# Kernel tuning notes

Measured on AMD Instinct MI355X. Metric: run time of the kernel, lower is better.

The kernel has to match this reference:

```python
import jax, jax.numpy as jnp
import numpy as np

N, L, E_Q, E_TOTAL, H, FORECAST = 4, 2048, 512, 512, 8, 8
E_HEAD = E_TOTAL // H
DT = 1.0
NEG = -1e30


def setup_inputs() -> dict:
    rng = jax.random.key(0)
    ks = jax.random.split(rng, 8)
    inv = 1.0 / np.sqrt(E_Q)
    return {
        "query": jax.random.normal(ks[0], (N, L, E_Q), jnp.float32),
        "key": jax.random.normal(ks[1], (N, L, E_Q), jnp.float32),
        "value": jax.random.normal(ks[2], (N, L, E_Q), jnp.float32),
        "Wqkv": jax.random.normal(ks[3], (E_Q, 3 * E_TOTAL), jnp.float32) * inv,
        "bqkv": jnp.zeros((3 * E_TOTAL,), jnp.float32),
        "Wo": jax.random.normal(ks[4], (E_TOTAL, E_Q), jnp.float32) * (1.0 / np.sqrt(E_TOTAL)),
        "bo": jnp.zeros((E_Q,), jnp.float32),
        "Xi": jax.random.normal(ks[5], (H, E_HEAD, E_HEAD), jnp.float32) * 0.02,
    }


def reference(query, key, value, Wqkv, bqkv, Wo, bo, Xi):
    # NOTE: original forward projects `query` into q,k,v (key/value args unused).
    b, s, _ = query.shape
    qkv = query @ Wqkv + bqkv                      # [b, s, 3E]
    q, k, v = jnp.split(qkv, 3, axis=-1)
    split_heads = lambda t: t.reshape(b, s, H, E_HEAD).transpose(0, 2, 1, 3)  # [b,H,s,h]
    q, k, v = split_heads(q), split_heads(k), split_heads(v)
    # causal SDPA
    scale = 1.0 / np.sqrt(E_HEAD)
    scores = jnp.einsum('bhqd,bhkd->bhqk', q, k) * scale
    causal = jnp.tril(jnp.ones((s, s), bool))
    scores = jnp.where(causal, scores, NEG)
    probs = jax.nn.softmax(scores, axis=-1)
    attn = jnp.einsum('bhqk,bhkd->bhqd', probs, v)  # [b,H,s,h]
    # per-head SINDy linear dynamics, strict symmetry -> skew-symmetric A
    A = Xi - jnp.swapaxes(Xi, -1, -2)               # [H,h,h]

    def step(x, _):
        x2 = x + DT * jnp.einsum('bhsd,hde->bhse', x, A)
        return x2, x2

    _, ys = jax.lax.scan(step, attn, None, length=FORECAST)  # [n,b,H,s,h]
    roll = jnp.transpose(ys, (1, 0, 3, 2, 4)).reshape(b, FORECAST, s, E_TOTAL)
    return roll @ Wo + bo                            # [b, n, s, E_q]
```

## Files before the change

kernel.cpp:

```cpp
#include <hip/hip_runtime.h>
#include <math.h>


#define NEGV -1e30f

typedef __bf16 bf16_t;
typedef __bf16 bf16x4 __attribute__((ext_vector_type(4)));
typedef __bf16 bf16x8 __attribute__((ext_vector_type(8)));
typedef float f32x4 __attribute__((ext_vector_type(4)));
typedef unsigned u32x4 __attribute__((ext_vector_type(4)));

#define MFMA(a, b, c) __builtin_amdgcn_mfma_f32_16x16x32_bf16((a), (b), (c), 0, 0, 0)

#define QSCALE 0.18033688011112042f

__device__ __forceinline__ bf16x8* swz_ptr(bf16_t* base, int r, int cb) {
  return (bf16x8*)((char*)base + r * 128 + (cb ^ ((r & 7) << 4)));
}
__device__ __forceinline__ const bf16x8* swz_cptr(const bf16_t* base, int r, int cb) {
  return (const bf16x8*)((const char*)base + r * 128 + (cb ^ ((r & 7) << 4)));
}

__device__ __forceinline__ void gload16(const bf16_t* g, bf16_t* l) {
  __builtin_amdgcn_global_load_lds(
      (const __attribute__((address_space(1))) void*)g,
      (__attribute__((address_space(3))) void*)l, 16, 0, 0);
}

__device__ __forceinline__ unsigned cvt_pk_bf16(float lo, float hi) {
  unsigned r;
  asm("v_cvt_pk_bf16_f32 %0, %1, %2" : "=v"(r) : "v"(lo), "v"(hi));
  return r;
}


__global__ __launch_bounds__(256) void prep(const float* __restrict__ X,
                                            const float* __restrict__ W,
                                            const float* __restrict__ Xi,
                                            bf16_t* __restrict__ Xb,
                                            bf16_t* __restrict__ WT,
                                            float* __restrict__ pows) {
  __shared__ __align__(16) char smem[2 * 64 * 68 * 4];
  const int bx = blockIdx.x;
  const int tid = threadIdx.x;
  if (bx < 8) {
    const int h = bx;
    float (*P)[68] = (float(*)[68])smem;
    float (*cur)[68] = (float(*)[68])(smem + 64 * 68 * 4);
    const float* xi = Xi + (size_t)h * 4096;
    float* dst = pows + (size_t)h * 8 * 4096;
    for (int idx = tid; idx < 4096; idx += 256) {
      const int i = idx >> 6, j = idx & 63;
      const float p = (i == j ? 1.f : 0.f) + xi[i * 64 + j] - xi[j * 64 + i];
      P[i][j] = p;
      cur[i][j] = p;
      dst[idx] = p;
    }
    __syncthreads();
    const int i = tid >> 2;
    const int j0 = (tid & 3) * 16;
    for (int n = 1; n < 8; ++n) {
      float a[16];
#pragma unroll
      for (int jj = 0; jj < 16; ++jj) a[jj] = 0.f;
      for (int dd = 0; dd < 64; ++dd) {
        const float c = cur[i][dd];
#pragma unroll
        for (int jj = 0; jj < 16; ++jj) a[jj] += c * P[dd][j0 + jj];
      }
      __syncthreads();
#pragma unroll
      for (int jj = 0; jj < 16; ++jj) {
        cur[i][j0 + jj] = a[jj];
        dst[n * 4096 + i * 64 + j0 + jj] = a[jj];
      }
      __syncthreads();
    }
  } else if (bx < 200) {
    const int idx = bx - 8;
    const int n0 = (idx % 24) * 64, k0 = (idx / 24) * 64;
    float (*Wf)[65] = (float(*)[65])smem;
#pragma unroll
    for (int c = 0; c < 16; ++c) {
      const int id2 = tid + c * 256;
      const int kk = id2 >> 6, nn = id2 & 63;
      Wf[kk][nn] = W[(size_t)(k0 + kk) * 1536 + n0 + nn];
    }
    __syncthreads();
    const int nr = tid >> 2;
    const int jb = (tid & 3) * 2;
#pragma unroll
    for (int t = 0; t < 2; ++t) {
      const int j = jb + t;
      bf16x8 v;
#pragma unroll
      for (int i = 0; i < 8; ++i) v[i] = (bf16_t)Wf[j * 8 + i][nr];
      *(bf16x8*)&WT[(size_t)(n0 + nr) * 512 + k0 + 8 * (j ^ (nr & 7))] = v;
    }
  } else {
    const int gid = (bx - 200) * 256 + tid;
    const int s = gid >> 6, j = gid & 63;
    const float4* src = (const float4*)(X + (size_t)s * 512 + j * 8);
    const float4 f0 = src[0], f1 = src[1];
    bf16x8 v;
    v[0] = (bf16_t)f0.x; v[1] = (bf16_t)f0.y; v[2] = (bf16_t)f0.z; v[3] = (bf16_t)f0.w;
    v[4] = (bf16_t)f1.x; v[5] = (bf16_t)f1.y; v[6] = (bf16_t)f1.z; v[7] = (bf16_t)f1.w;
    *(bf16x8*)&Xb[(size_t)s * 512 + (j >> 3) * 64 + 8 * ((j & 7) ^ (s & 7))] = v;
  }
}

__global__ __launch_bounds__(256) void build_B(const float* __restrict__ pows,
                                               const float* __restrict__ Wo,
                                               bf16_t* __restrict__ BmatT) {
  const int et = blockIdx.x;
  const int n = blockIdx.y;
  const int h = blockIdx.z;
  __shared__ __align__(16) float P[64][68];
  __shared__ __align__(16) float We[64][128];
  const int tid = threadIdx.x;
  const float* src = pows + ((size_t)h * 8 + n) * 4096;
  for (int idx = tid; idx < 4096; idx += 256) P[idx >> 6][idx & 63] = src[idx];
  const int e0 = et * 128;
  for (int idx = tid; idx < 8192; idx += 256) {
    const int dd = idx >> 7, e = idx & 127;
    We[dd][e] = Wo[(size_t)(h * 64 + dd) * 512 + e0 + e];
  }
  __syncthreads();
  const int d = tid >> 2;
  const int eq = (tid & 3) * 32;
  float acc[32];
#pragma unroll
  for (int j = 0; j < 32; ++j) acc[j] = 0.f;
  for (int dd = 0; dd < 64; ++dd) {
    const float p = P[d][dd];
#pragma unroll
    for (int j = 0; j < 32; ++j) acc[j] += p * We[dd][eq + j];
  }
  bf16_t* dst = BmatT + (size_t)n * 512 * 512 + (size_t)(e0 + eq) * 512 + h * 64;
  const int dlo = d & 7, dhi = d >> 3;
#pragma unroll
  for (int j = 0; j < 32; ++j)
    dst[(size_t)j * 512 + 8 * (dhi ^ (j & 7)) + dlo] = (bf16_t)acc[j];
}

__global__ __launch_bounds__(256) void qkv_gemm(const bf16_t* __restrict__ Xb,
                                                const bf16_t* __restrict__ WT,
                                                const float* __restrict__ bias,
                                                bf16_t* __restrict__ qw,
                                                bf16_t* __restrict__ kw,
                                                bf16_t* __restrict__ vt) {
  __shared__ __align__(16) bf16_t As[2][128 * 64];
  __shared__ __align__(16) bf16_t Bs[2][128 * 64];
  const int tid = threadIdx.x;
  const int wave = tid >> 6, lane = tid & 63;
  const int g = lane >> 4, li = lane & 15;
  const int row0 = blockIdx.x * 128;
  const int col0 = blockIdx.y * 128;
  const int wm = (wave >> 1) * 64, wn = (wave & 1) * 64;
  f32x4 acc[4][4] = {};
  const bf16_t* asrc = Xb + (size_t)(row0 + wave * 32 + (lane >> 3)) * 512 + (lane & 7) * 8;
  const bf16_t* bsrc = WT + (size_t)(col0 + wave * 32 + (lane >> 3)) * 512 + (lane & 7) * 8;
  bf16_t* adst0 = &As[0][wave * 32 * 64];
  bf16_t* adst1 = &As[1][wave * 32 * 64];
  bf16_t* bdst0 = &Bs[0][wave * 32 * 64];
  bf16_t* bdst1 = &Bs[1][wave * 32 * 64];
  auto stage = [&](int bi, int kt) {
    const int k0 = kt * 64;
    bf16_t* ad = bi ? adst1 : adst0;
    bf16_t* bd = bi ? bdst1 : bdst0;
#pragma unroll
    for (int c = 0; c < 4; ++c) {
      gload16(asrc + (size_t)c * 8 * 512 + k0, ad + c * 512);
      gload16(bsrc + (size_t)c * 8 * 512 + k0, bd + c * 512);
    }
  };
  stage(0, 0);
#pragma unroll
  for (int t = 0; t < 8; ++t) {
    const int cur = t & 1;
    if (t < 7) {
      stage(cur ^ 1, t + 1);
      asm volatile("s_waitcnt vmcnt(8)" ::: "memory");
    } else {
      asm volatile("s_waitcnt vmcnt(0)" ::: "memory");
    }
    __builtin_amdgcn_s_barrier();
    __builtin_amdgcn_sched_barrier(0);
#pragma unroll
    for (int ks = 0; ks < 2; ++ks) {
      bf16x8 af[4], bfr[4];
#pragma unroll
      for (int mr = 0; mr < 4; ++mr)
        af[mr] = *swz_cptr(As[cur], wm + mr * 16 + li, ks * 64 + g * 16);
#pragma unroll
      for (int nr = 0; nr < 4; ++nr)
        bfr[nr] = *swz_cptr(Bs[cur], wn + nr * 16 + li, ks * 64 + g * 16);
#pragma unroll
      for (int mr = 0; mr < 4; ++mr)
#pragma unroll
        for (int nr = 0; nr < 4; ++nr)
          acc[mr][nr] = MFMA(af[mr], bfr[nr], acc[mr][nr]);
    }
    __builtin_amdgcn_s_barrier();
    __builtin_amdgcn_sched_barrier(0);
  }
  const int cbase = col0 + wn;
  const int sel = cbase >> 9;
  const int hh = (cbase & 511) >> 6;
  const int bb = row0 >> 11;
  const size_t hb = (size_t)(bb * 8 + hh) * (2048 * 64);
  if (sel == 2) {
    bf16_t* vbase = vt + hb;
#pragma unroll
    for (int nr = 0; nr < 4; ++nr) {
      const int dcol = nr * 16 + li;
      const float bv = bias[cbase + dcol];
#pragma unroll
      for (int mr = 0; mr < 4; ++mr) {
        bf16x4 pk;
#pragma unroll
        for (int i = 0; i < 4; ++i) pk[i] = (bf16_t)(acc[mr][nr][i] + bv);
        const int s = (row0 + wm + mr * 16 + g * 4) & 2047;
        *(bf16x4*)&vbase[(size_t)dcol * 2048 + s] = pk;
      }
    }
  } else {
    bf16_t* dstp = (sel == 0 ? qw : kw) + hb;
    const float sc = (sel == 0) ? QSCALE : 1.0f;
#pragma unroll
    for (int nr = 0; nr < 4; ++nr) {
      const int dcol = nr * 16 + li;
      const float bv = bias[cbase + dcol];
#pragma unroll
      for (int mr = 0; mr < 4; ++mr) {
#pragma unroll
        for (int i = 0; i < 4; ++i) {
          const int r = row0 + wm + mr * 16 + g * 4 + i;
          const int s = r & 2047;
          dstp[(size_t)s * 64 + dcol] = (bf16_t)((acc[mr][nr][i] + bv) * sc);
        }
      }
    }
  }
}

__global__ __launch_bounds__(256) void fattn(const bf16_t* __restrict__ qw,
                                             const bf16_t* __restrict__ kw,
                                             const bf16_t* __restrict__ vt,
                                             bf16_t* __restrict__ attn,
                                             float* __restrict__ opart,
                                             float* __restrict__ ml) {
  __shared__ __align__(16) bf16_t Ks[2][64][64];
  __shared__ __align__(16) bf16_t Vs[2][64][64];
  const int tid = threadIdx.x;
  const int w = tid >> 6;
  const int lane = tid & 63;
  const int g = lane >> 4;
  const int li = lane & 15;
  const int x = blockIdx.x;
  int qt, ktb, kte, chunk;
  bool split;
  if (x < 16) {
    qt = 31 - x; ktb = 0; kte = 16; chunk = 0; split = true;
  } else if (x < 32) {
    qt = 47 - x; ktb = 16; kte = qt + 1; chunk = 1; split = true;
  } else {
    qt = 47 - x; ktb = 0; kte = qt + 1; chunk = 0; split = false;
  }
  const int h = blockIdx.y;
  const int b = blockIdx.z;
  const size_t base = ((size_t)(b * 8 + h)) * (2048 * 64);
  const int q0 = qt * 64;
  const int qrow = q0 + w * 16 + li;
  const bf16x8 aq0 = *(const bf16x8*)(qw + base + (size_t)qrow * 64 + g * 8);
  const bf16x8 aq1 = *(const bf16x8*)(qw + base + (size_t)qrow * 64 + 32 + g * 8);
  const bf16_t* kbase = kw + base;
  const bf16_t* vbase = vt + base;
  const int r_st = tid >> 2;
  const int qu = tid & 3;
  {
    const bf16_t* kp = kbase + (size_t)(ktb * 64 + r_st) * 64 + qu * 16;
    const bf16_t* vp = vbase + (size_t)r_st * 2048 + ktb * 64 + qu * 16;
    *swz_ptr(&Ks[0][0][0], r_st, qu * 32) = *(const bf16x8*)kp;
    *swz_ptr(&Ks[0][0][0], r_st, qu * 32 + 16) = *(const bf16x8*)(kp + 8);
    *swz_ptr(&Vs[0][0][0], r_st, qu * 32) = *(const bf16x8*)vp;
    *swz_ptr(&Vs[0][0][0], r_st, qu * 32 + 16) = *(const bf16x8*)(vp + 8);
  }
  f32x4 accO[4] = {};
  float m_run = -__builtin_inff();
  float l_run = 0.f;
  for (int kt = ktb; kt < kte; ++kt) {
    __syncthreads();
    const int cur = (kt - ktb) & 1;
    const bool pf = (kt + 1) < kte;
    bf16x8 nk0, nk1, nv0, nv1;
    if (pf) {
      const int kb2 = (kt + 1) * 64;
      const bf16_t* kp = kbase + (size_t)(kb2 + r_st) * 64 + qu * 16;
      const bf16_t* vp = vbase + (size_t)r_st * 2048 + kb2 + qu * 16;
      nk0 = *(const bf16x8*)kp;
      nk1 = *(const bf16x8*)(kp + 8);
      nv0 = *(const bf16x8*)vp;
      nv1 = *(const bf16x8*)(vp + 8);
    }
    f32x4 sv[4];
    __builtin_amdgcn_s_setprio(1);
#pragma unroll
    for (int nt = 0; nt < 4; ++nt) {
      const bf16x8 bk0 = *swz_cptr(&Ks[cur][0][0], nt * 16 + li, g * 16);
      const bf16x8 bk1 = *swz_cptr(&Ks[cur][0][0], nt * 16 + li, 64 + g * 16);
      f32x4 z = {0.f, 0.f, 0.f, 0.f};
      z = MFMA(bk0, aq0, z);
      sv[nt] = MFMA(bk1, aq1, z);
    }
    __builtin_amdgcn_s_setprio(0);
    if (kt == qt) {
#pragma unroll
      for (int nt = 0; nt < 4; ++nt)
#pragma unroll
        for (int i = 0; i < 4; ++i)
          if (nt * 16 + g * 4 + i > w * 16 + li) sv[nt][i] = NEGV;
    }
    float pmax = sv[0][0];
#pragma unroll
    for (int nt = 0; nt < 4; ++nt)
#pragma unroll
      for (int i = 0; i < 4; ++i) pmax = fmaxf(pmax, sv[nt][i]);
    pmax = fmaxf(pmax, __shfl_xor(pmax, 16, 64));
    pmax = fmaxf(pmax, __shfl_xor(pmax, 32, 64));
    if (!__all(pmax - m_run <= 8.f)) {
      const float newm = fmaxf(m_run, pmax);
      const float sc = exp2f(m_run - newm);
      l_run *= sc;
      m_run = newm;
#pragma unroll
      for (int nt = 0; nt < 4; ++nt)
#pragma unroll
        for (int i = 0; i < 4; ++i) accO[nt][i] *= sc;
    }
    float rsum = 0.f;
#pragma unroll
    for (int nt = 0; nt < 4; ++nt) {
#pragma unroll
      for (int i = 0; i < 4; ++i) {
        const float p = exp2f(sv[nt][i] - m_run);
        sv[nt][i] = p;
        rsum += p;
      }
    }
    rsum += __shfl_xor(rsum, 16, 64);
    rsum += __shfl_xor(rsum, 32, 64);
    l_run += rsum;
    const unsigned pk00 = cvt_pk_bf16(sv[0][0], sv[0][1]);
    const unsigned pk01 = cvt_pk_bf16(sv[0][2], sv[0][3]);
    const unsigned pk10 = cvt_pk_bf16(sv[1][0], sv[1][1]);
    const unsigned pk11 = cvt_pk_bf16(sv[1][2], sv[1][3]);
    const unsigned pk20 = cvt_pk_bf16(sv[2][0], sv[2][1]);
    const unsigned pk21 = cvt_pk_bf16(sv[2][2], sv[2][3]);
    const unsigned pk30 = cvt_pk_bf16(sv[3][0], sv[3][1]);
    const unsigned pk31 = cvt_pk_bf16(sv[3][2], sv[3][3]);
    bf16x8 ap0, ap1;
    {
      auto s0 = __builtin_amdgcn_permlane32_swap((int)pk00, (int)pk10, false, false);
      auto t0 = __builtin_amdgcn_permlane16_swap(s0[0], s0[1], false, false);
      auto s1 = __builtin_amdgcn_permlane32_swap((int)pk01, (int)pk11, false, false);
      auto t1 = __builtin_amdgcn_permlane16_swap(s1[0], s1[1], false, false);
      u32x4 wd = {(unsigned)t0[0], (unsigned)t1[0], (unsigned)t0[1], (unsigned)t1[1]};
      ap0 = __builtin_bit_cast(bf16x8, wd);
    }
    {
      auto s0 = __builtin_amdgcn_permlane32_swap((int)pk20, (int)pk30, false, false);
      auto t0 = __builtin_amdgcn_permlane16_swap(s0[0], s0[1], false, false);
      auto s1 = __builtin_amdgcn_permlane32_swap((int)pk21, (int)pk31, false, false);
      auto t1 = __builtin_amdgcn_permlane16_swap(s1[0], s1[1], false, false);
      u32x4 wd = {(unsigned)t0[0], (unsigned)t1[0], (unsigned)t0[1], (unsigned)t1[1]};
      ap1 = __builtin_bit_cast(bf16x8, wd);
    }
    __builtin_amdgcn_s_setprio(1);
#pragma unroll
    for (int nt = 0; nt < 4; ++nt) {
      const bf16x8 bv0 = *swz_cptr(&Vs[cur][0][0], nt * 16 + li, g * 16);
      const bf16x8 bv1 = *swz_cptr(&Vs[cur][0][0], nt * 16 + li, 64 + g * 16);
      accO[nt] = MFMA(bv0, ap0, accO[nt]);
      accO[nt] = MFMA(bv1, ap1, accO[nt]);
    }
    __builtin_amdgcn_s_setprio(0);
    if (pf) {
      *swz_ptr(&Ks[cur ^ 1][0][0], r_st, qu * 32) = nk0;
      *swz_ptr(&Ks[cur ^ 1][0][0], r_st, qu * 32 + 16) = nk1;
      *swz_ptr(&Vs[cur ^ 1][0][0], r_st, qu * 32) = nv0;
      *swz_ptr(&Vs[cur ^ 1][0][0], r_st, qu * 32 + 16) = nv1;
    }
  }
  if (!split) {
    const float inv = 1.0f / l_run;
    bf16_t* arow = attn + (size_t)(b * 2048 + qrow) * 512 + h * 64;
#pragma unroll
    for (int nt = 0; nt < 4; ++nt) {
      bf16x4 pk;
#pragma unroll
      for (int i = 0; i < 4; ++i) pk[i] = (bf16_t)(accO[nt][i] * inv);
      *(bf16x4*)&arow[8 * ((nt * 2 + (g >> 1)) ^ (li & 7)) + (g & 1) * 4] = pk;
    }
  } else {
    const int row = w * 16 + li;
    const size_t pbase = (((size_t)(b * 8 + h) * 16 + (qt - 16)) * 2 + chunk) * 64 + row;
    float* op = opart + pbase * 64;
#pragma unroll
    for (int nt = 0; nt < 4; ++nt) *(f32x4*)&op[nt * 16 + g * 4] = accO[nt];
    if (g == 0) {
      ml[pbase * 2] = m_run;
      ml[pbase * 2 + 1] = l_run;
    }
  }
}

__global__ __launch_bounds__(256) void fcombine(const float* __restrict__ opart,
                                                const float* __restrict__ ml,
                                                bf16_t* __restrict__ attn) {
  const int qi = blockIdx.x;
  const int h = blockIdx.y;
  const int b = blockIdx.z;
  const int tid = threadIdx.x;
  const int row = tid >> 2;
  const int dq = (tid & 3) * 16;
  const size_t base2 = ((size_t)(b * 8 + h) * 16 + qi) * 2;
  const size_t p0 = (base2 * 64 + row);
  const size_t p1 = ((base2 + 1) * 64 + row);
  const float m1 = ml[p0 * 2], l1 = ml[p0 * 2 + 1];
  const float m2 = ml[p1 * 2], l2 = ml[p1 * 2 + 1];
  const float m = fmaxf(m1, m2);
  const float w1 = exp2f(m1 - m), w2 = exp2f(m2 - m);
  const float inv = 1.0f / (l1 * w1 + l2 * w2);
  const float* o1 = opart + p0 * 64;
  const float* o2 = opart + p1 * 64;
  const int qrow = (16 + qi) * 64 + row;
  bf16_t* arow = attn + (size_t)(b * 2048 + qrow) * 512 + h * 64;
#pragma unroll
  for (int t = 0; t < 2; ++t) {
    const int c0 = dq + t * 8;
    const f32x4 a1 = *(const f32x4*)&o1[c0];
    const f32x4 b1 = *(const f32x4*)&o1[c0 + 4];
    const f32x4 a2 = *(const f32x4*)&o2[c0];
    const f32x4 b2 = *(const f32x4*)&o2[c0 + 4];
    bf16x8 v;
#pragma unroll
    for (int i = 0; i < 4; ++i) {
      v[i] = (bf16_t)((a1[i] * w1 + a2[i] * w2) * inv);
      v[4 + i] = (bf16_t)((b1[i] * w1 + b2[i] * w2) * inv);
    }
    *(bf16x8*)&arow[8 * ((c0 >> 3) ^ (row & 7))] = v;
  }
}

__global__ __launch_bounds__(256) void out_gemm(const bf16_t* __restrict__ A,
                                                const bf16_t* __restrict__ BmatT,
                                                const float* __restrict__ bo,
                                                float* __restrict__ out) {
  __shared__ __align__(16) bf16_t As[2][128 * 64];
  const int tid = threadIdx.x;
  const int wave = tid >> 6, lane = tid & 63;
  const int g = lane >> 4, li = lane & 15;
  const int row0 = blockIdx.x * 128;
  const int col0 = blockIdx.y * 128;
  const int nf = blockIdx.z;
  const int wm = (wave >> 1) * 64, wn = (wave & 1) * 64;
  f32x4 acc[4][4] = {};
  const bf16_t* asrc = A + (size_t)(row0 + wave * 32 + (lane >> 3)) * 512 + (lane & 7) * 8;
  bf16_t* adst0 = &As[0][wave * 32 * 64];
  bf16_t* adst1 = &As[1][wave * 32 * 64];
  const char* Bnf = (const char*)(BmatT + (size_t)nf * 512 * 512);
  unsigned boff[2][4];
#pragma unroll
  for (int ks = 0; ks < 2; ++ks)
#pragma unroll
    for (int nr = 0; nr < 4; ++nr) {
      const int row = col0 + wn + nr * 16 + li;
      boff[ks][nr] = (unsigned)(row * 1024 + 16 * ((ks * 4 + g) ^ (row & 7)));
    }
  auto stageA = [&](int bi, int kt) {
    bf16_t* ad = bi ? adst1 : adst0;
#pragma unroll
    for (int c = 0; c < 4; ++c)
      gload16(asrc + (size_t)c * 8 * 512 + kt * 64, ad + c * 512);
  };
  bf16x8 bfr[2][2][4];
  auto loadB = [&](int bi, int kt) {
#pragma unroll
    for (int ks = 0; ks < 2; ++ks)
#pragma unroll
      for (int nr = 0; nr < 4; ++nr)
        bfr[bi][ks][nr] = *(const bf16x8*)(Bnf + boff[ks][nr] + kt * 128);
  };
  stageA(0, 0);
  loadB(0, 0);
#pragma unroll
  for (int t = 0; t < 8; ++t) {
    const int cur = t & 1;
    if (t < 7) {
      stageA(cur ^ 1, t + 1);
      loadB(cur ^ 1, t + 1);
      asm volatile("s_waitcnt vmcnt(12)" ::: "memory");
    } else {
      asm volatile("s_waitcnt vmcnt(0)" ::: "memory");
    }
    __builtin_amdgcn_s_barrier();
    __builtin_amdgcn_sched_barrier(0);
#pragma unroll
    for (int ks = 0; ks < 2; ++ks) {
      bf16x8 af[4];
#pragma unroll
      for (int mr = 0; mr < 4; ++mr)
        af[mr] = *swz_cptr(As[cur], wm + mr * 16 + li, ks * 64 + g * 16);
#pragma unroll
      for (int mr = 0; mr < 4; ++mr)
#pragma unroll
        for (int nr = 0; nr < 4; ++nr)
          acc[mr][nr] = MFMA(af[mr], bfr[cur][ks][nr], acc[mr][nr]);
    }
    __builtin_amdgcn_s_barrier();
    __builtin_amdgcn_sched_barrier(0);
  }
  const int bb = row0 >> 11;
  float* obase = out + ((size_t)(bb * 8 + nf)) * (2048 * 512);
#pragma unroll
  for (int nr = 0; nr < 4; ++nr) {
    const int c = col0 + wn + nr * 16 + li;
    const float bv = bo[c];
#pragma unroll
    for (int mr = 0; mr < 4; ++mr) {
#pragma unroll
      for (int i = 0; i < 4; ++i) {
        const int r = row0 + wm + mr * 16 + g * 4 + i;
        const int s = r & 2047;
        __builtin_nontemporal_store(acc[mr][nr][i] + bv, &obase[(size_t)s * 512 + c]);
      }
    }
  }
}

extern "C" void kernel_launch(void* const* d_in, const int* in_sizes, int n_in,
                              void* d_out, int out_size, void* d_ws, size_t ws_size,
                              hipStream_t stream) {
  const float* query = (const float*)d_in[0];
  const float* Wqkv = (const float*)d_in[3];
  const float* bqkv = (const float*)d_in[4];
  const float* Wo = (const float*)d_in[5];
  const float* bo = (const float*)d_in[6];
  const float* Xi = (const float*)d_in[7];
  float* out = (float*)d_out;

  char* ws = (char*)d_ws;
  bf16_t* qw = (bf16_t*)(ws + 0);
  bf16_t* kw = (bf16_t*)(ws + 8388608);
  bf16_t* vt = (bf16_t*)(ws + 16777216);
  bf16_t* Xb = (bf16_t*)(ws + 25165824);
  bf16_t* attn = (bf16_t*)(ws + 25165824);
  bf16_t* BmatT = (bf16_t*)(ws + 33554432);
  float* pows = (float*)(ws + 37748736);
  bf16_t* WT = (bf16_t*)(ws + 38797312);
  float* opart = (float*)(ws + 40370176);
  float* mlbuf = (float*)(ws + 57147392);

  prep<<<dim3(2248), dim3(256), 0, stream>>>(query, Wqkv, Xi, Xb, WT, pows);
  build_B<<<dim3(4, 8, 8), dim3(256), 0, stream>>>(pows, Wo, BmatT);
  qkv_gemm<<<dim3(64, 12), dim3(256), 0, stream>>>(Xb, WT, bqkv, qw, kw, vt);
  fattn<<<dim3(48, 8, 4), dim3(256), 0, stream>>>(qw, kw, vt, attn, opart, mlbuf);
  fcombine<<<dim3(16, 8, 4), dim3(256), 0, stream>>>(opart, mlbuf, attn);
  out_gemm<<<dim3(64, 4, 8), dim3(256), 0, stream>>>(attn, BmatT, bo, out);
}
```

Baseline: 181.1 us.

## Process 128 query rows per attention block to reuse K/V tiles across two row groups

```diff
diff --git a/kernel.cpp b/kernel.cpp
--- a/kernel.cpp
+++ b/kernel.cpp
@@ -258,22 +258,26 @@
   const int g = lane >> 4;
   const int li = lane & 15;
   const int x = blockIdx.x;
-  int qt, ktb, kte, chunk;
+  int qt2, ktb, kte, chunk;
   bool split;
-  if (x < 16) {
-    qt = 31 - x; ktb = 0; kte = 16; chunk = 0; split = true;
-  } else if (x < 32) {
-    qt = 47 - x; ktb = 16; kte = qt + 1; chunk = 1; split = true;
+  if (x < 8) {
+    qt2 = 15 - x; ktb = 0; kte = qt2 + 1; chunk = 0; split = true;
+  } else if (x < 16) {
+    qt2 = 23 - x; ktb = qt2 + 1; kte = 2 * qt2 + 2; chunk = 1; split = true;
   } else {
-    qt = 47 - x; ktb = 0; kte = qt + 1; chunk = 0; split = false;
+    qt2 = 23 - x; ktb = 0; kte = 2 * qt2 + 2; chunk = 0; split = false;
   }
   const int h = blockIdx.y;
   const int b = blockIdx.z;
   const size_t base = ((size_t)(b * 8 + h)) * (2048 * 64);
-  const int q0 = qt * 64;
-  const int qrow = q0 + w * 16 + li;
-  const bf16x8 aq0 = *(const bf16x8*)(qw + base + (size_t)qrow * 64 + g * 8);
-  const bf16x8 aq1 = *(const bf16x8*)(qw + base + (size_t)qrow * 64 + 32 + g * 8);
+  const int rbase0 = qt2 * 128 + w * 32;
+  bf16x8 aq[2][2];
+#pragma unroll
+  for (int u = 0; u < 2; ++u) {
+    const bf16_t* qp = qw + base + (size_t)(rbase0 + u * 16 + li) * 64 + g * 8;
+    aq[u][0] = *(const bf16x8*)qp;
+    aq[u][1] = *(const bf16x8*)(qp + 32);
+  }
   const bf16_t* kbase = kw + base;
   const bf16_t* vbase = vt + base;
   const int r_st = tid >> 2;
@@ -286,16 +290,17 @@
     *swz_ptr(&Vs[0][0][0], r_st, qu * 32) = *(const bf16x8*)vp;
     *swz_ptr(&Vs[0][0][0], r_st, qu * 32 + 16) = *(const bf16x8*)(vp + 8);
   }
-  f32x4 accO[4] = {};
-  float m_run = -__builtin_inff();
-  float l_run = 0.f;
+  f32x4 accO[2][4] = {};
+  float m_run[2] = {-__builtin_inff(), -__builtin_inff()};
+  float l_run[2] = {0.f, 0.f};
   for (int kt = ktb; kt < kte; ++kt) {
     __syncthreads();
     const int cur = (kt - ktb) & 1;
     const bool pf = (kt + 1) < kte;
+    const int kb = kt * 64;
     bf16x8 nk0, nk1, nv0, nv1;
     if (pf) {
-      const int kb2 = (kt + 1) * 64;
+      const int kb2 = kb + 64;
       const bf16_t* kp = kbase + (size_t)(kb2 + r_st) * 64 + qu * 16;
       const bf16_t* vp = vbase + (size_t)r_st * 2048 + kb2 + qu * 16;
       nk0 = *(const bf16x8*)kp;
@@ -303,88 +308,97 @@
       nv0 = *(const bf16x8*)vp;
       nv1 = *(const bf16x8*)(vp + 8);
     }
-    f32x4 sv[4];
-    __builtin_amdgcn_s_setprio(1);
+    bf16x8 bk[8];
 #pragma unroll
     for (int nt = 0; nt < 4; ++nt) {
-      const bf16x8 bk0 = *swz_cptr(&Ks[cur][0][0], nt * 16 + li, g * 16);
-      const bf16x8 bk1 = *swz_cptr(&Ks[cur][0][0], nt * 16 + li, 64 + g * 16);
-      f32x4 z = {0.f, 0.f, 0.f, 0.f};
-      z = MFMA(bk0, aq0, z);
-      sv[nt] = MFMA(bk1, aq1, z);
-    }
-    __builtin_amdgcn_s_setprio(0);
-    if (kt == qt) {
+      bk[2 * nt] = *swz_cptr(&Ks[cur][0][0], nt * 16 + li, g * 16);
+      bk[2 * nt + 1] = *swz_cptr(&Ks[cur][0][0], nt * 16 + li, 64 + g * 16);
+    }
+#pragma unroll
+    for (int u = 0; u < 2; ++u) {
+      const int rbase = rbase0 + u * 16;
+      if (kb > rbase + 15) continue;
+      f32x4 sv[4];
+      __builtin_amdgcn_s_setprio(1);
+#pragma unroll
+      for (int nt = 0; nt < 4; ++nt) {
+        f32x4 z = {0.f, 0.f, 0.f, 0.f};
+        z = MFMA(bk[2 * nt], aq[u][0], z);
+        sv[nt] = MFMA(bk[2 * nt + 1], aq[u][1], z);
+      }
+      __builtin_amdgcn_s_setprio(0);
+      if (kb + 63 > rbase) {
+#pragma unroll
+        for (int nt = 0; nt < 4; ++nt)
+#pragma unroll
+          for (int i = 0; i < 4; ++i)
+            if (kb + nt * 16 + g * 4 + i > rbase + li) sv[nt][i] = NEGV;
+      }
+      float pmax = sv[0][0];
 #pragma unroll
       for (int nt = 0; nt < 4; ++nt)
 #pragma unroll
-        for (int i = 0; i < 4; ++i)
-          if (nt * 16 + g * 4 + i > w * 16 + li) sv[nt][i] = NEGV;
-    }
-    float pmax = sv[0][0];
-#pragma unroll
-    for (int nt = 0; nt < 4; ++nt)
-#pragma unroll
-      for (int i = 0; i < 4; ++i) pmax = fmaxf(pmax, sv[nt][i]);
-    pmax = fmaxf(pmax, __shfl_xor(pmax, 16, 64));
-    pmax = fmaxf(pmax, __shfl_xor(pmax, 32, 64));
-    if (!__all(pmax - m_run <= 8.f)) {
-      const float newm = fmaxf(m_run, pmax);
-      const float sc = exp2f(m_run - newm);
-      l_run *= sc;
-      m_run = newm;
-#pragma unroll
-      for (int nt = 0; nt < 4; ++nt)
-#pragma unroll
-        for (int i = 0; i < 4; ++i) accO[nt][i] *= sc;
-    }
-    float rsum = 0.f;
-#pragma unroll
-    for (int nt = 0; nt < 4; ++nt) {
-#pragma unroll
-      for (int i = 0; i < 4; ++i) {
-        const float p = exp2f(sv[nt][i] - m_run);
-        sv[nt][i] = p;
-        rsum += p;
-      }
-    }
-    rsum += __shfl_xor(rsum, 16, 64);
-    rsum += __shfl_xor(rsum, 32, 64);
-    l_run += rsum;
-    const unsigned pk00 = cvt_pk_bf16(sv[0][0], sv[0][1]);
-    const unsigned pk01 = cvt_pk_bf16(sv[0][2], sv[0][3]);
-    const unsigned pk10 = cvt_pk_bf16(sv[1][0], sv[1][1]);
-    const unsigned pk11 = cvt_pk_bf16(sv[1][2], sv[1][3]);
-    const unsigned pk20 = cvt_pk_bf16(sv[2][0], sv[2][1]);
-    const unsigned pk21 = cvt_pk_bf16(sv[2][2], sv[2][3]);
-    const unsigned pk30 = cvt_pk_bf16(sv[3][0], sv[3][1]);
-    const unsigned pk31 = cvt_pk_bf16(sv[3][2], sv[3][3]);
-    bf16x8 ap0, ap1;
-    {
-      auto s0 = __builtin_amdgcn_permlane32_swap((int)pk00, (int)pk10, false, false);
-      auto t0 = __builtin_amdgcn_permlane16_swap(s0[0], s0[1], false, false);
-      auto s1 = __builtin_amdgcn_permlane32_swap((int)pk01, (int)pk11, false, false);
-      auto t1 = __builtin_amdgcn_permlane16_swap(s1[0], s1[1], false, false);
-      u32x4 wd = {(unsigned)t0[0], (unsigned)t1[0], (unsigned)t0[1], (unsigned)t1[1]};
-      ap0 = __builtin_bit_cast(bf16x8, wd);
-    }
-    {
-      auto s0 = __builtin_amdgcn_permlane32_swap((int)pk20, (int)pk30, false, false);
-      auto t0 = __builtin_amdgcn_permlane16_swap(s0[0], s0[1], false, false);
-      auto s1 = __builtin_amdgcn_permlane32_swap((int)pk21, (int)pk31, false, false);
-      auto t1 = __builtin_amdgcn_permlane16_swap(s1[0], s1[1], false, false);
-      u32x4 wd = {(unsigned)t0[0], (unsigned)t1[0], (unsigned)t0[1], (unsigned)t1[1]};
-      ap1 = __builtin_bit_cast(bf16x8, wd);
-    }
-    __builtin_amdgcn_s_setprio(1);
-#pragma unroll
-    for (int nt = 0; nt < 4; ++nt) {
-      const bf16x8 bv0 = *swz_cptr(&Vs[cur][0][0], nt * 16 + li, g * 16);
-      const bf16x8 bv1 = *swz_cptr(&Vs[cur][0][0], nt * 16 + li, 64 + g * 16);
-      accO[nt] = MFMA(bv0, ap0, accO[nt]);
-      accO[nt] = MFMA(bv1, ap1, accO[nt]);
-    }
-    __builtin_amdgcn_s_setprio(0);
+        for (int i = 0; i < 4; ++i) pmax = fmaxf(pmax, sv[nt][i]);
+      pmax = fmaxf(pmax, __shfl_xor(pmax, 16, 64));
+      pmax = fmaxf(pmax, __shfl_xor(pmax, 32, 64));
+      if (!__all(pmax - m_run[u] <= 8.f)) {
+        const float newm = fmaxf(m_run[u], pmax);
+        const float sc = exp2f(m_run[u] - newm);
+        l_run[u] *= sc;
+        m_run[u] = newm;
+#pragma unroll
+        for (int nt = 0; nt < 4; ++nt)
+#pragma unroll
+          for (int i = 0; i < 4; ++i) accO[u][nt][i] *= sc;
+      }
+      float rsum = 0.f;
+#pragma unroll
+      for (int nt = 0; nt < 4; ++nt) {
+#pragma unroll
+        for (int i = 0; i < 4; ++i) {
+          const float p = exp2f(sv[nt][i] - m_run[u]);
+          sv[nt][i] = p;
+          rsum += p;
+        }
+      }
+      rsum += __shfl_xor(rsum, 16, 64);
+      rsum += __shfl_xor(rsum, 32, 64);
+      l_run[u] += rsum;
+      const unsigned pk00 = cvt_pk_bf16(sv[0][0], sv[0][1]);
+      const unsigned pk01 = cvt_pk_bf16(sv[0][2], sv[0][3]);
+      const unsigned pk10 = cvt_pk_bf16(sv[1][0], sv[1][1]);
+      const unsigned pk11 = cvt_pk_bf16(sv[1][2], sv[1][3]);
+      const unsigned pk20 = cvt_pk_bf16(sv[2][0], sv[2][1]);
+      const unsigned pk21 = cvt_pk_bf16(sv[2][2], sv[2][3]);
+      const unsigned pk30 = cvt_pk_bf16(sv[3][0], sv[3][1]);
+      const unsigned pk31 = cvt_pk_bf16(sv[3][2], sv[3][3]);
+      bf16x8 ap0, ap1;
+      {
+        auto s0 = __builtin_amdgcn_permlane32_swap((int)pk00, (int)pk10, false, false);
+        auto t0 = __builtin_amdgcn_permlane16_swap(s0[0], s0[1], false, false);
+        auto s1 = __builtin_amdgcn_permlane32_swap((int)pk01, (int)pk11, false, false);
+        auto t1 = __builtin_amdgcn_permlane16_swap(s1[0], s1[1], false, false);
+        u32x4 wd = {(unsigned)t0[0], (unsigned)t1[0], (unsigned)t0[1], (unsigned)t1[1]};
+        ap0 = __builtin_bit_cast(bf16x8, wd);
+      }
+      {
+        auto s0 = __builtin_amdgcn_permlane32_swap((int)pk20, (int)pk30, false, false);
+        auto t0 = __builtin_amdgcn_permlane16_swap(s0[0], s0[1], false, false);
+        auto s1 = __builtin_amdgcn_permlane32_swap((int)pk21, (int)pk31, false, false);
+        auto t1 = __builtin_amdgcn_permlane16_swap(s1[0], s1[1], false, false);
+        u32x4 wd = {(unsigned)t0[0], (unsigned)t1[0], (unsigned)t0[1], (unsigned)t1[1]};
+        ap1 = __builtin_bit_cast(bf16x8, wd);
+      }
+      __builtin_amdgcn_s_setprio(1);
+#pragma unroll
+      for (int nt = 0; nt < 4; ++nt) {
+        const bf16x8 bv0 = *swz_cptr(&Vs[cur][0][0], nt * 16 + li, g * 16);
+        const bf16x8 bv1 = *swz_cptr(&Vs[cur][0][0], nt * 16 + li, 64 + g * 16);
+        accO[u][nt] = MFMA(bv0, ap0, accO[u][nt]);
+        accO[u][nt] = MFMA(bv1, ap1, accO[u][nt]);
+      }
+      __builtin_amdgcn_s_setprio(0);
+    }
     if (pf) {
       *swz_ptr(&Ks[cur ^ 1][0][0], r_st, qu * 32) = nk0;
       *swz_ptr(&Ks[cur ^ 1][0][0], r_st, qu * 32 + 16) = nk1;
@@ -393,24 +407,31 @@
     }
   }
   if (!split) {
-    const float inv = 1.0f / l_run;
-    bf16_t* arow = attn + (size_t)(b * 2048 + qrow) * 512 + h * 64;
-#pragma unroll
-    for (int nt = 0; nt < 4; ++nt) {
-      bf16x4 pk;
-#pragma unroll
-      for (int i = 0; i < 4; ++i) pk[i] = (bf16_t)(accO[nt][i] * inv);
-      *(bf16x4*)&arow[8 * ((nt * 2 + (g >> 1)) ^ (li & 7)) + (g & 1) * 4] = pk;
+#pragma unroll
+    for (int u = 0; u < 2; ++u) {
+      const float inv = 1.0f / l_run[u];
+      bf16_t* arow = attn + (size_t)(b * 2048 + rbase0 + u * 16 + li) * 512 + h * 64;
+#pragma unroll
+      for (int nt = 0; nt < 4; ++nt) {
+        bf16x4 pk;
+#pragma unroll
+        for (int i = 0; i < 4; ++i) pk[i] = (bf16_t)(accO[u][nt][i] * inv);
+        *(bf16x4*)&arow[8 * ((nt * 2 + (g >> 1)) ^ (li & 7)) + (g & 1) * 4] = pk;
+      }
     }
   } else {
-    const int row = w * 16 + li;
-    const size_t pbase = (((size_t)(b * 8 + h) * 16 + (qt - 16)) * 2 + chunk) * 64 + row;
-    float* op = opart + pbase * 64;
-#pragma unroll
-    for (int nt = 0; nt < 4; ++nt) *(f32x4*)&op[nt * 16 + g * 4] = accO[nt];
-    if (g == 0) {
-      ml[pbase * 2] = m_run;
-      ml[pbase * 2 + 1] = l_run;
+#pragma unroll
+    for (int u = 0; u < 2; ++u) {
+      const int row = w * 32 + u * 16 + li;
+      const size_t pbase =
+          (((size_t)(b * 8 + h) * 8 + (qt2 - 8)) * 2 + chunk) * 128 + row;
+      float* op = opart + pbase * 64;
+#pragma unroll
+      for (int nt = 0; nt < 4; ++nt) *(f32x4*)&op[nt * 16 + g * 4] = accO[u][nt];
+      if (g == 0) {
+        ml[pbase * 2] = m_run[u];
+        ml[pbase * 2 + 1] = l_run[u];
+      }
     }
   }
 }
@@ -419,14 +440,17 @@
                                                 const float* __restrict__ ml,
                                                 bf16_t* __restrict__ attn) {
   const int qi = blockIdx.x;
+  const int qt2i = qi >> 1;
+  const int rowoff = (qi & 1) * 64;
   const int h = blockIdx.y;
   const int b = blockIdx.z;
   const int tid = threadIdx.x;
   const int row = tid >> 2;
   const int dq = (tid & 3) * 16;
-  const size_t base2 = ((size_t)(b * 8 + h) * 16 + qi) * 2;
-  const size_t p0 = (base2 * 64 + row);
-  const size_t p1 = ((base2 + 1) * 64 + row);
+  const int prow = rowoff + row;
+  const size_t base2 = ((size_t)(b * 8 + h) * 8 + qt2i) * 2;
+  const size_t p0 = base2 * 128 + prow;
+  const size_t p1 = (base2 + 1) * 128 + prow;
   const float m1 = ml[p0 * 2], l1 = ml[p0 * 2 + 1];
   const float m2 = ml[p1 * 2], l2 = ml[p1 * 2 + 1];
   const float m = fmaxf(m1, m2);
@@ -434,7 +458,7 @@
   const float inv = 1.0f / (l1 * w1 + l2 * w2);
   const float* o1 = opart + p0 * 64;
   const float* o2 = opart + p1 * 64;
-  const int qrow = (16 + qi) * 64 + row;
+  const int qrow = (8 + qt2i) * 128 + prow;
   bf16_t* arow = attn + (size_t)(b * 2048 + qrow) * 512 + h * 64;
 #pragma unroll
   for (int t = 0; t < 2; ++t) {
@@ -565,7 +589,7 @@
   prep<<<dim3(2248), dim3(256), 0, stream>>>(query, Wqkv, Xi, Xb, WT, pows);
   build_B<<<dim3(4, 8, 8), dim3(256), 0, stream>>>(pows, Wo, BmatT);
   qkv_gemm<<<dim3(64, 12), dim3(256), 0, stream>>>(Xb, WT, bqkv, qw, kw, vt);
-  fattn<<<dim3(48, 8, 4), dim3(256), 0, stream>>>(qw, kw, vt, attn, opart, mlbuf);
+  fattn<<<dim3(24, 8, 4), dim3(256), 0, stream>>>(qw, kw, vt, attn, opart, mlbuf);
   fcombine<<<dim3(16, 8, 4), dim3(256), 0, stream>>>(opart, mlbuf, attn);
   out_gemm<<<dim3(64, 4, 8), dim3(256), 0, stream>>>(attn, BmatT, bo, out);
 }
```

Measured after the change: 197.8 us. 9.2% more time.
